# Performance work log

Hardware: AMD Instinct MI355X
Metric: run time of the kernel (lower is better)

Reference implementation:

```python
import jax, jax.numpy as jnp
import numpy as np

N = 100000       # nodes
E = 3200000      # edges (avg degree 32)
IN_F = 256
OUT_F = 128
LRELU_ALPHA = 0.2
EPS = 1e-16


def setup_inputs() -> dict:
    key = jax.random.key(0)
    k1, k2, k3, k4 = jax.random.split(key, 4)
    x = jax.random.normal(k1, (N, IN_F), dtype=jnp.float32)
    edge_index = jax.random.randint(k2, (2, E), 0, N, dtype=jnp.int32)
    # xavier_uniform with gain=calculate_gain('relu')=sqrt(2)
    gain = float(np.sqrt(2.0))
    bw = gain * float(np.sqrt(6.0 / (IN_F + OUT_F)))
    weight = jax.random.uniform(k3, (IN_F, OUT_F), dtype=jnp.float32, minval=-bw, maxval=bw)
    ba = gain * float(np.sqrt(6.0 / (1 + 2 * OUT_F)))
    a = jax.random.uniform(k4, (1, 2 * OUT_F), dtype=jnp.float32, minval=-ba, maxval=ba)
    return {"x": x, "edge_index": edge_index, "weight": weight, "a": a}


def reference(x, edge_index, weight, a):
    src = edge_index[0]
    dst = edge_index[1]
    h = x @ weight                                  # [N, OUT_F]
    # e_edge = a @ cat(h[src], h[dst]) == (h @ a_l)[src] + (h @ a_r)[dst]
    a_l = a[0, :OUT_F]
    a_r = a[0, OUT_F:]
    s_l = h @ a_l                                   # [N]
    s_r = h @ a_r                                   # [N]
    e = s_l[src] + s_r[dst]                         # [E]
    e = jnp.where(e >= 0, e, LRELU_ALPHA * e)       # LeakyReLU
    # segment softmax over src groups
    e_max = jax.ops.segment_max(e, src, num_segments=N)   # [N]
    e_exp = jnp.exp(e - e_max[src])                        # [E]
    denom = jax.ops.segment_sum(e_exp, src, num_segments=N)[src] + EPS
    alpha_e = e_exp / denom                                # [E]
    # out[src] += alpha_e * h[dst]  (sparse A_alpha @ h)
    out = jax.ops.segment_sum(alpha_e[:, None] * h[dst], src, num_segments=N)
    return out
```

## Files before the change

kernel.cpp:

```cpp
#include <hip/hip_runtime.h>

#define GN 100000
#define GE 3200000
#define CAP 128
#define NB 391
#define CHUNK 4096

typedef __attribute__((ext_vector_type(8))) short bf16x8;
typedef __attribute__((ext_vector_type(4))) float f32x4;

__device__ __forceinline__ unsigned short f2bf(float f) {
    unsigned u = __float_as_uint(f);
    u += 0x7fffu + ((u >> 16) & 1u);
    return (unsigned short)(u >> 16);
}
__device__ __forceinline__ float bf2f(unsigned short u) {
    return __uint_as_float(((unsigned)u) << 16);
}

__global__ __launch_bounds__(256) void wprep_kernel(const float* __restrict__ w,
                                                    unsigned short* __restrict__ wT) {
    int flat4 = blockIdx.x * 256 + threadIdx.x;
    if (flat4 >= 256 * 128 / 4) return;
    int k  = flat4 >> 5;
    int n4 = (flat4 & 31) * 4;
    float4 v = ((const float4*)w)[flat4];
    wT[(size_t)(n4 + 0) * 256 + k] = f2bf(v.x);
    wT[(size_t)(n4 + 1) * 256 + k] = f2bf(v.y);
    wT[(size_t)(n4 + 2) * 256 + k] = f2bf(v.z);
    wT[(size_t)(n4 + 3) * 256 + k] = f2bf(v.w);
}

__global__ __launch_bounds__(256) void gemm_kernel(const float* __restrict__ x,
                                                   const unsigned short* __restrict__ wT,
                                                   const float* __restrict__ a,
                                                   unsigned short* __restrict__ hq,
                                                   float* __restrict__ s_l,
                                                   float* __restrict__ s_r) {
    __shared__ unsigned short As[128][40];
    const int tid  = threadIdx.x;
    const int lane = tid & 63, wid = tid >> 6;
    const int l16  = lane & 15, quad = lane >> 4;
    const int wm   = (wid >> 1) * 64, wn = (wid & 1) * 64;
    const int bm   = blockIdx.x * 128;

    f32x4 acc[4][4] = {};

    const int arow = tid >> 1, ahalf = tid & 1;
    int gr = bm + arow; if (gr >= GN) gr = GN - 1;
    const float* xrow = x + (size_t)gr * 256 + ahalf * 16;

    for (int k0 = 0; k0 < 256; k0 += 32) {
        float4 f0 = *(const float4*)(xrow + k0);
        float4 f1 = *(const float4*)(xrow + k0 + 4);
        float4 f2 = *(const float4*)(xrow + k0 + 8);
        float4 f3 = *(const float4*)(xrow + k0 + 12);
        bf16x8 s0, s1;
        s0[0] = f2bf(f0.x); s0[1] = f2bf(f0.y); s0[2] = f2bf(f0.z); s0[3] = f2bf(f0.w);
        s0[4] = f2bf(f1.x); s0[5] = f2bf(f1.y); s0[6] = f2bf(f1.z); s0[7] = f2bf(f1.w);
        s1[0] = f2bf(f2.x); s1[1] = f2bf(f2.y); s1[2] = f2bf(f2.z); s1[3] = f2bf(f2.w);
        s1[4] = f2bf(f3.x); s1[5] = f2bf(f3.y); s1[6] = f2bf(f3.z); s1[7] = f2bf(f3.w);
        __syncthreads();
        *(bf16x8*)&As[arow][ahalf * 16]     = s0;
        *(bf16x8*)&As[arow][ahalf * 16 + 8] = s1;
        __syncthreads();
        bf16x8 af[4], bfr[4];
#pragma unroll
        for (int t = 0; t < 4; ++t) {
            af[t]  = *(const bf16x8*)&As[wm + t * 16 + l16][quad * 8];
            bfr[t] = *(const bf16x8*)(wT + (size_t)(wn + t * 16 + l16) * 256 + k0 + quad * 8);
        }
#pragma unroll
        for (int ti = 0; ti < 4; ++ti)
#pragma unroll
            for (int tj = 0; tj < 4; ++tj)
                acc[ti][tj] = __builtin_amdgcn_mfma_f32_16x16x32_bf16(af[ti], bfr[tj], acc[ti][tj], 0, 0, 0);
    }

    float alv[4], arv[4];
#pragma unroll
    for (int tj = 0; tj < 4; ++tj) {
        alv[tj] = a[wn + tj * 16 + l16];
        arv[tj] = a[128 + wn + tj * 16 + l16];
    }
#pragma unroll
    for (int ti = 0; ti < 4; ++ti) {
        float slp[4], srp[4];
#pragma unroll
        for (int r = 0; r < 4; ++r) {
            int row = bm + wm + ti * 16 + quad * 4 + r;
            float v0 = acc[ti][0][r], v1 = acc[ti][1][r], v2 = acc[ti][2][r], v3 = acc[ti][3][r];
            if (row < GN) {
                unsigned short* hp = hq + (size_t)row * 128 + wn + l16;
                hp[0]  = f2bf(v0);
                hp[16] = f2bf(v1);
                hp[32] = f2bf(v2);
                hp[48] = f2bf(v3);
            }
            slp[r] = v0 * alv[0] + v1 * alv[1] + v2 * alv[2] + v3 * alv[3];
            srp[r] = v0 * arv[0] + v1 * arv[1] + v2 * arv[2] + v3 * arv[3];
        }
#pragma unroll
        for (int off = 1; off < 16; off <<= 1)
#pragma unroll
            for (int r = 0; r < 4; ++r) {
                slp[r] += __shfl_xor(slp[r], off, 64);
                srp[r] += __shfl_xor(srp[r], off, 64);
            }
        if (l16 == 0) {
#pragma unroll
            for (int r = 0; r < 4; ++r) {
                int row = bm + wm + ti * 16 + quad * 4 + r;
                if (row < GN) {
                    atomicAdd(&s_l[row], slp[r]);
                    atomicAdd(&s_r[row], srp[r]);
                }
            }
        }
    }
}

__global__ __launch_bounds__(256) void bhist_kernel(const int* __restrict__ src,
                                                    int* __restrict__ bcnt) {
    __shared__ int bh[NB];
    const int tid = threadIdx.x;
    for (int j = tid; j < NB; j += 256) bh[j] = 0;
    __syncthreads();
    const int base = blockIdx.x * CHUNK;
    const int cnt = min(CHUNK, GE - base);
    for (int i = tid; i < cnt; i += 256) atomicAdd(&bh[src[base + i] >> 8], 1);
    __syncthreads();
    for (int j = tid; j < NB; j += 256)
        if (bh[j]) atomicAdd(&bcnt[j], bh[j]);
}

__global__ __launch_bounds__(64) void bscan_kernel(const int* __restrict__ bcnt,
                                                   int* __restrict__ bbase,
                                                   int* __restrict__ bcursor) {
    __shared__ int arr[NB];
    const int tid = threadIdx.x;
    for (int j = tid; j < NB; j += 64) arr[j] = bcnt[j];
    __syncthreads();
    int carry = 0;
    for (int b0 = 0; b0 < NB; b0 += 64) {
        int idx = b0 + tid;
        int v = (idx < NB) ? arr[idx] : 0;
        int x = v;
#pragma unroll
        for (int off = 1; off < 64; off <<= 1) {
            int y = __shfl_up(x, off, 64);
            if (tid >= off) x += y;
        }
        if (idx < NB) { bbase[idx] = carry + x - v; bcursor[idx] = carry + x - v; }
        carry += __shfl(x, 63, 64);
    }
    if (tid == 0) bbase[NB] = carry;
}

__global__ __launch_bounds__(256) void bin_kernel(const int* __restrict__ ei,
                                                  int* __restrict__ bcursor,
                                                  unsigned* __restrict__ binned) {
    __shared__ int h_cnt[NB];
    __shared__ int h_base[NB + 1];
    __shared__ int h_gpos[NB];
    __shared__ int h_cur[NB];
    __shared__ unsigned sbuf[CHUNK];
    const int tid = threadIdx.x;
    const int base = blockIdx.x * CHUNK;
    const int cnt = min(CHUNK, GE - base);

    int srcv[CHUNK / 256], dstv[CHUNK / 256];
#pragma unroll
    for (int i = 0; i < CHUNK / 256; ++i) {
        int idx = tid + i * 256;
        if (idx < cnt) { srcv[i] = ei[base + idx]; dstv[i] = ei[GE + base + idx]; }
        else srcv[i] = -1;
    }
    for (int j = tid; j < NB; j += 256) h_cnt[j] = 0;
    __syncthreads();
#pragma unroll
    for (int i = 0; i < CHUNK / 256; ++i)
        if (srcv[i] >= 0) atomicAdd(&h_cnt[srcv[i] >> 8], 1);
    __syncthreads();
    if (tid < 64) {
        int carry = 0;
        for (int b0 = 0; b0 < NB; b0 += 64) {
            int idx = b0 + tid;
            int v = (idx < NB) ? h_cnt[idx] : 0;
            int x = v;
#pragma unroll
            for (int off = 1; off < 64; off <<= 1) {
                int y = __shfl_up(x, off, 64);
                if (tid >= off) x += y;
            }
            if (idx < NB) h_base[idx] = carry + x - v;
            carry += __shfl(x, 63, 64);
        }
        if (tid == 0) h_base[NB] = carry;
    }
    __syncthreads();
    for (int j = tid; j < NB; j += 256) {
        h_cur[j] = h_base[j];
        int c = h_cnt[j];
        if (c) h_gpos[j] = atomicAdd(&bcursor[j], c);
    }
    __syncthreads();
#pragma unroll
    for (int i = 0; i < CHUNK / 256; ++i)
        if (srcv[i] >= 0) {
            int b = srcv[i] >> 8;
            int p = atomicAdd(&h_cur[b], 1);
            sbuf[p] = ((unsigned)(srcv[i] & 255) << 17) | (unsigned)dstv[i];
        }
    __syncthreads();
    for (int p = tid; p < cnt; p += 256) {
        int lo = 0, hi = NB - 1;
        while (lo < hi) {
            int mid = (lo + hi + 1) >> 1;
            if (h_base[mid] <= p) lo = mid; else hi = mid - 1;
        }
        binned[h_gpos[lo] + (p - h_base[lo])] = sbuf[p];
    }
}

__global__ __launch_bounds__(256) void fine_kernel(const unsigned* __restrict__ binned,
                                                   const int* __restrict__ bbase,
                                                   int* __restrict__ rowptr,
                                                   int* __restrict__ adj) {
    __shared__ int n_cnt[256];
    __shared__ int n_base[257];
    __shared__ int n_cur[256];
    const int b = blockIdx.x;
    const int tid = threadIdx.x;
    const int node0 = b * 256;
    const int nn = min(256, GN - node0);
    const int beg = bbase[b], end = bbase[b + 1];
    n_cnt[tid] = 0;
    __syncthreads();
    for (int p = beg + tid; p < end; p += 256)
        atomicAdd(&n_cnt[binned[p] >> 17], 1);
    __syncthreads();
    if (tid < 64) {
        int carry = 0;
        for (int b0 = 0; b0 < 256; b0 += 64) {
            int idx = b0 + tid;
            int v = n_cnt[idx];
            int x = v;
#pragma unroll
            for (int off = 1; off < 64; off <<= 1) {
                int y = __shfl_up(x, off, 64);
                if (tid >= off) x += y;
            }
            n_base[idx] = carry + x - v;
            carry += __shfl(x, 63, 64);
        }
        if (tid == 0) n_base[256] = carry;
    }
    __syncthreads();
    if (tid < nn) rowptr[node0 + tid] = beg + n_base[tid];
    if (b == NB - 1 && tid == 0) rowptr[GN] = end;
    n_cur[tid] = n_base[tid];
    __syncthreads();
    for (int p = beg + tid; p < end; p += 256) {
        unsigned e = binned[p];
        int s = e >> 17, d = (int)(e & 0x1FFFFu);
        int pos = atomicAdd(&n_cur[s], 1);
        adj[beg + pos] = d;
    }
}

__global__ __launch_bounds__(256) void aggregate_kernel(const ushort2* __restrict__ h2,
                                                        const float* __restrict__ s_l,
                                                        const float* __restrict__ s_r,
                                                        const int* __restrict__ rowptr,
                                                        const int* __restrict__ adj,
                                                        float* __restrict__ out) {
    __shared__ int   s_dst[4][CAP];
    __shared__ float s_al[4][CAP];
    const int wid = threadIdx.x >> 6, lane = threadIdx.x & 63;
    const int node = blockIdx.x * 4 + wid;
    const int beg = rowptr[node], end = rowptr[node + 1];
    const int deg = end - beg;
    const float sl = s_l[node];

    float m = -1e30f, d = 0.f;
    for (int j = lane; j < deg; j += 64) {
        int dst = adj[beg + j];
        float e = sl + s_r[dst];
        e = (e >= 0.f) ? e : 0.2f * e;
        if (j < CAP) { s_dst[wid][j] = dst; s_al[wid][j] = e; }
        float mn = fmaxf(m, e);
        d = d * __expf(m - mn) + __expf(e - mn);
        m = mn;
    }
#pragma unroll
    for (int off = 32; off; off >>= 1) {
        float m2 = __shfl_xor(m, off, 64);
        float d2 = __shfl_xor(d, off, 64);
        float mn = fmaxf(m, m2);
        d = d * __expf(m - mn) + d2 * __expf(m2 - mn);
        m = mn;
    }
    float inv = 1.f / (d + 1e-16f);
    __syncthreads();
    const int n2 = deg < CAP ? deg : CAP;
    for (int j = lane; j < n2; j += 64)
        s_al[wid][j] = __expf(s_al[wid][j] - m) * inv;
    __syncthreads();

    float2 acc = {0.f, 0.f};
    int j = 0;
    for (; j + 4 <= n2; j += 4) {
        int   d0 = s_dst[wid][j],      d1 = s_dst[wid][j + 1];
        int   d2i = s_dst[wid][j + 2], d3 = s_dst[wid][j + 3];
        float a0 = s_al[wid][j],       a1 = s_al[wid][j + 1];
        float a2 = s_al[wid][j + 2],   a3 = s_al[wid][j + 3];
        ushort2 v0 = h2[(size_t)d0 * 64 + lane];
        ushort2 v1 = h2[(size_t)d1 * 64 + lane];
        ushort2 v2 = h2[(size_t)d2i * 64 + lane];
        ushort2 v3 = h2[(size_t)d3 * 64 + lane];
        acc.x += a0 * bf2f(v0.x) + a1 * bf2f(v1.x) + a2 * bf2f(v2.x) + a3 * bf2f(v3.x);
        acc.y += a0 * bf2f(v0.y) + a1 * bf2f(v1.y) + a2 * bf2f(v2.y) + a3 * bf2f(v3.y);
    }
    for (; j < n2; ++j) {
        int d0 = s_dst[wid][j]; float a0 = s_al[wid][j];
        ushort2 v0 = h2[(size_t)d0 * 64 + lane];
        acc.x += a0 * bf2f(v0.x); acc.y += a0 * bf2f(v0.y);
    }
    for (; j < deg; ++j) {
        int dst = adj[beg + j];
        float e = sl + s_r[dst];
        e = (e >= 0.f) ? e : 0.2f * e;
        float a0 = __expf(e - m) * inv;
        ushort2 v0 = h2[(size_t)dst * 64 + lane];
        acc.x += a0 * bf2f(v0.x); acc.y += a0 * bf2f(v0.y);
    }
    ((float2*)out)[(size_t)node * 64 + lane] = acc;
}

extern "C" void kernel_launch(void* const* d_in, const int* in_sizes, int n_in,
                              void* d_out, int out_size, void* d_ws, size_t ws_size,
                              hipStream_t stream) {
    const float* x  = (const float*)d_in[0];
    const int*   ei = (const int*)d_in[1];
    const float* w  = (const float*)d_in[2];
    const float* a  = (const float*)d_in[3];
    float* out = (float*)d_out;

    unsigned short* hq = (unsigned short*)d_ws;
    float* s_l     = (float*)(hq + (size_t)GN * 128);
    float* s_r     = s_l + GN;
    int*   bcnt    = (int*)(s_r + GN);
    int*   bbase   = bcnt + NB;
    int*   bcursor = bbase + NB + 1;
    int*   rowptr  = bcursor + NB;
    unsigned* binned = (unsigned*)(rowptr + GN + 1);
    int*   adj     = (int*)(binned + GE);
    unsigned short* wT = (unsigned short*)(adj + GE);

    hipMemsetAsync(s_l, 0, (size_t)(2 * GN + NB) * sizeof(float), stream);

    wprep_kernel<<<32, 256, 0, stream>>>(w, wT);
    gemm_kernel<<<(GN + 127) / 128, 256, 0, stream>>>(x, wT, a, hq, s_l, s_r);
    bhist_kernel<<<(GE + CHUNK - 1) / CHUNK, 256, 0, stream>>>(ei, bcnt);
    bscan_kernel<<<1, 64, 0, stream>>>(bcnt, bbase, bcursor);
    bin_kernel<<<(GE + CHUNK - 1) / CHUNK, 256, 0, stream>>>(ei, bcursor, binned);
    fine_kernel<<<NB, 256, 0, stream>>>(binned, bbase, rowptr, adj);
    aggregate_kernel<<<GN / 4, 256, 0, stream>>>((const ushort2*)hq, s_l, s_r, rowptr, adj, out);
}
```

Before: 412.7 us.

## Switch to fp16 storage, finer bins, bucket tags, restructured aggregate

Several changes land together. h and W move from bf16 to fp16, using packed RTZ conversion and f16 MFMA. The bin count doubles to 782 (128 nodes per bin), so fine_kernel gets more, smaller blocks. bin_kernel stores each entry's bucket id in shared memory, which replaces a per-element binary search. The aggregate kernel becomes a two-pass max-then-sum softmax that stores (dst, alpha) pairs together, gathers half4 values with half-wave splitting over two edges, and defers normalization to the end. It keeps a separate fallback path for high-degree nodes. fp16 has a narrower range than bf16 and could overflow on large h values.

```diff
diff --git a/kernel.cpp b/kernel.cpp
--- a/kernel.cpp
+++ b/kernel.cpp
@@ -3,41 +3,39 @@
 #define GN 100000
 #define GE 3200000
 #define CAP 128
-#define NB 391
+#define NB 782
 #define CHUNK 4096
 
-typedef __attribute__((ext_vector_type(8))) short bf16x8;
+typedef __attribute__((ext_vector_type(8))) _Float16 f16x8;
+typedef __attribute__((ext_vector_type(4))) _Float16 half4_t;
+typedef __attribute__((ext_vector_type(2))) __fp16 fp16x2_raw;
 typedef __attribute__((ext_vector_type(4))) float f32x4;
 
-__device__ __forceinline__ unsigned short f2bf(float f) {
-    unsigned u = __float_as_uint(f);
-    u += 0x7fffu + ((u >> 16) & 1u);
-    return (unsigned short)(u >> 16);
-}
-__device__ __forceinline__ float bf2f(unsigned short u) {
-    return __uint_as_float(((unsigned)u) << 16);
+__device__ __forceinline__ unsigned pk2(float a, float b) {
+    fp16x2_raw p = __builtin_amdgcn_cvt_pkrtz(a, b);
+    return __builtin_bit_cast(unsigned, p);
 }
 
 __global__ __launch_bounds__(256) void wprep_kernel(const float* __restrict__ w,
-                                                    unsigned short* __restrict__ wT) {
+                                                    _Float16* __restrict__ wT) {
     int flat4 = blockIdx.x * 256 + threadIdx.x;
     if (flat4 >= 256 * 128 / 4) return;
     int k  = flat4 >> 5;
     int n4 = (flat4 & 31) * 4;
     float4 v = ((const float4*)w)[flat4];
-    wT[(size_t)(n4 + 0) * 256 + k] = f2bf(v.x);
-    wT[(size_t)(n4 + 1) * 256 + k] = f2bf(v.y);
-    wT[(size_t)(n4 + 2) * 256 + k] = f2bf(v.z);
-    wT[(size_t)(n4 + 3) * 256 + k] = f2bf(v.w);
+    wT[(size_t)(n4 + 0) * 256 + k] = (_Float16)v.x;
+    wT[(size_t)(n4 + 1) * 256 + k] = (_Float16)v.y;
+    wT[(size_t)(n4 + 2) * 256 + k] = (_Float16)v.z;
+    wT[(size_t)(n4 + 3) * 256 + k] = (_Float16)v.w;
 }
 
 __global__ __launch_bounds__(256) void gemm_kernel(const float* __restrict__ x,
-                                                   const unsigned short* __restrict__ wT,
+                                                   const _Float16* __restrict__ wT,
                                                    const float* __restrict__ a,
-                                                   unsigned short* __restrict__ hq,
+                                                   _Float16* __restrict__ hq,
                                                    float* __restrict__ s_l,
                                                    float* __restrict__ s_r) {
-    __shared__ unsigned short As[128][40];
+    __shared__ _Float16 As[128][40];
     const int tid  = threadIdx.x;
     const int lane = tid & 63, wid = tid >> 6;
     const int l16  = lane & 15, quad = lane >> 4;
@@ -55,26 +53,23 @@
         float4 f1 = *(const float4*)(xrow + k0 + 4);
         float4 f2 = *(const float4*)(xrow + k0 + 8);
         float4 f3 = *(const float4*)(xrow + k0 + 12);
-        bf16x8 s0, s1;
-        s0[0] = f2bf(f0.x); s0[1] = f2bf(f0.y); s0[2] = f2bf(f0.z); s0[3] = f2bf(f0.w);
-        s0[4] = f2bf(f1.x); s0[5] = f2bf(f1.y); s0[6] = f2bf(f1.z); s0[7] = f2bf(f1.w);
-        s1[0] = f2bf(f2.x); s1[1] = f2bf(f2.y); s1[2] = f2bf(f2.z); s1[3] = f2bf(f2.w);
-        s1[4] = f2bf(f3.x); s1[5] = f2bf(f3.y); s1[6] = f2bf(f3.z); s1[7] = f2bf(f3.w);
+        uint4 lo = {pk2(f0.x, f0.y), pk2(f0.z, f0.w), pk2(f1.x, f1.y), pk2(f1.z, f1.w)};
+        uint4 hi = {pk2(f2.x, f2.y), pk2(f2.z, f2.w), pk2(f3.x, f3.y), pk2(f3.z, f3.w)};
         __syncthreads();
-        *(bf16x8*)&As[arow][ahalf * 16]     = s0;
-        *(bf16x8*)&As[arow][ahalf * 16 + 8] = s1;
+        *(uint4*)&As[arow][ahalf * 16]     = lo;
+        *(uint4*)&As[arow][ahalf * 16 + 8] = hi;
         __syncthreads();
-        bf16x8 af[4], bfr[4];
+        f16x8 af[4], bfr[4];
 #pragma unroll
         for (int t = 0; t < 4; ++t) {
-            af[t]  = *(const bf16x8*)&As[wm + t * 16 + l16][quad * 8];
-            bfr[t] = *(const bf16x8*)(wT + (size_t)(wn + t * 16 + l16) * 256 + k0 + quad * 8);
+            af[t]  = *(const f16x8*)&As[wm + t * 16 + l16][quad * 8];
+            bfr[t] = *(const f16x8*)(wT + (size_t)(wn + t * 16 + l16) * 256 + k0 + quad * 8);
         }
 #pragma unroll
         for (int ti = 0; ti < 4; ++ti)
 #pragma unroll
             for (int tj = 0; tj < 4; ++tj)
-                acc[ti][tj] = __builtin_amdgcn_mfma_f32_16x16x32_bf16(af[ti], bfr[tj], acc[ti][tj], 0, 0, 0);
+                acc[ti][tj] = __builtin_amdgcn_mfma_f32_16x16x32_f16(af[ti], bfr[tj], acc[ti][tj], 0, 0, 0);
     }
 
     float alv[4], arv[4];
@@ -91,11 +86,11 @@
             int row = bm + wm + ti * 16 + quad * 4 + r;
             float v0 = acc[ti][0][r], v1 = acc[ti][1][r], v2 = acc[ti][2][r], v3 = acc[ti][3][r];
             if (row < GN) {
-                unsigned short* hp = hq + (size_t)row * 128 + wn + l16;
-                hp[0]  = f2bf(v0);
-                hp[16] = f2bf(v1);
-                hp[32] = f2bf(v2);
-                hp[48] = f2bf(v3);
+                _Float16* hp = hq + (size_t)row * 128 + wn + l16;
+                hp[0]  = (_Float16)v0;
+                hp[16] = (_Float16)v1;
+                hp[32] = (_Float16)v2;
+                hp[48] = (_Float16)v3;
             }
             slp[r] = v0 * alv[0] + v1 * alv[1] + v2 * alv[2] + v3 * alv[3];
             srp[r] = v0 * arv[0] + v1 * arv[1] + v2 * arv[2] + v3 * arv[3];
@@ -128,7 +123,7 @@
     __syncthreads();
     const int base = blockIdx.x * CHUNK;
     const int cnt = min(CHUNK, GE - base);
-    for (int i = tid; i < cnt; i += 256) atomicAdd(&bh[src[base + i] >> 8], 1);
+    for (int i = tid; i < cnt; i += 256) atomicAdd(&bh[src[base + i] >> 7], 1);
     __syncthreads();
     for (int j = tid; j < NB; j += 256)
         if (bh[j]) atomicAdd(&bcnt[j], bh[j]);
@@ -165,6 +160,7 @@
     __shared__ int h_gpos[NB];
     __shared__ int h_cur[NB];
     __shared__ unsigned sbuf[CHUNK];
+    __shared__ unsigned short bkt[CHUNK];
     const int tid = threadIdx.x;
     const int base = blockIdx.x * CHUNK;
     const int cnt = min(CHUNK, GE - base);
@@ -180,7 +176,7 @@
     __syncthreads();
 #pragma unroll
     for (int i = 0; i < CHUNK / 256; ++i)
-        if (srcv[i] >= 0) atomicAdd(&h_cnt[srcv[i] >> 8], 1);
+        if (srcv[i] >= 0) atomicAdd(&h_cnt[srcv[i] >> 7], 1);
     __syncthreads();
     if (tid < 64) {
         int carry = 0;
@@ -208,18 +204,15 @@
 #pragma unroll
     for (int i = 0; i < CHUNK / 256; ++i)
         if (srcv[i] >= 0) {
-            int b = srcv[i] >> 8;
+            int b = srcv[i] >> 7;
             int p = atomicAdd(&h_cur[b], 1);
-            sbuf[p] = ((unsigned)(srcv[i] & 255) << 17) | (unsigned)dstv[i];
+            sbuf[p] = ((unsigned)(srcv[i] & 127) << 17) | (unsigned)dstv[i];
+            bkt[p] = (unsigned short)b;
         }
     __syncthreads();
     for (int p = tid; p < cnt; p += 256) {
-        int lo = 0, hi = NB - 1;
-        while (lo < hi) {
-            int mid = (lo + hi + 1) >> 1;
-            if (h_base[mid] <= p) lo = mid; else hi = mid - 1;
-        }
-        binned[h_gpos[lo] + (p - h_base[lo])] = sbuf[p];
+        int b = bkt[p];
+        binned[h_gpos[b] + (p - h_base[b])] = sbuf[p];
     }
 }
 
@@ -227,22 +220,22 @@
                                                    const int* __restrict__ bbase,
                                                    int* __restrict__ rowptr,
                                                    int* __restrict__ adj) {
-    __shared__ int n_cnt[256];
-    __shared__ int n_base[257];
-    __shared__ int n_cur[256];
+    __shared__ int n_cnt[128];
+    __shared__ int n_base[129];
+    __shared__ int n_cur[128];
     const int b = blockIdx.x;
     const int tid = threadIdx.x;
-    const int node0 = b * 256;
-    const int nn = min(256, GN - node0);
+    const int node0 = b << 7;
+    const int nn = min(128, GN - node0);
     const int beg = bbase[b], end = bbase[b + 1];
-    n_cnt[tid] = 0;
+    if (tid < 128) n_cnt[tid] = 0;
     __syncthreads();
     for (int p = beg + tid; p < end; p += 256)
         atomicAdd(&n_cnt[binned[p] >> 17], 1);
     __syncthreads();
     if (tid < 64) {
         int carry = 0;
-        for (int b0 = 0; b0 < 256; b0 += 64) {
+        for (int b0 = 0; b0 < 128; b0 += 64) {
             int idx = b0 + tid;
             int v = n_cnt[idx];
             int x = v;
@@ -254,12 +247,12 @@
             n_base[idx] = carry + x - v;
             carry += __shfl(x, 63, 64);
         }
-        if (tid == 0) n_base[256] = carry;
+        if (tid == 0) n_base[128] = carry;
     }
     __syncthreads();
     if (tid < nn) rowptr[node0 + tid] = beg + n_base[tid];
     if (b == NB - 1 && tid == 0) rowptr[GN] = end;
-    n_cur[tid] = n_base[tid];
+    if (tid < 128) n_cur[tid] = n_base[tid];
     __syncthreads();
     for (int p = beg + tid; p < end; p += 256) {
         unsigned e = binned[p];
@@ -269,73 +262,96 @@
     }
 }
 
-__global__ __launch_bounds__(256) void aggregate_kernel(const ushort2* __restrict__ h2,
+__global__ __launch_bounds__(256) void aggregate_kernel(const half4_t* __restrict__ h4,
                                                         const float* __restrict__ s_l,
                                                         const float* __restrict__ s_r,
                                                         const int* __restrict__ rowptr,
                                                         const int* __restrict__ adj,
                                                         float* __restrict__ out) {
-    __shared__ int   s_dst[4][CAP];
-    __shared__ float s_al[4][CAP];
+    __shared__ uint2 s_ed[4][CAP + 4];
     const int wid = threadIdx.x >> 6, lane = threadIdx.x & 63;
     const int node = blockIdx.x * 4 + wid;
     const int beg = rowptr[node], end = rowptr[node + 1];
     const int deg = end - beg;
     const float sl = s_l[node];
 
-    float m = -1e30f, d = 0.f;
-    for (int j = lane; j < deg; j += 64) {
-        int dst = adj[beg + j];
-        float e = sl + s_r[dst];
-        e = (e >= 0.f) ? e : 0.2f * e;
-        if (j < CAP) { s_dst[wid][j] = dst; s_al[wid][j] = e; }
-        float mn = fmaxf(m, e);
-        d = d * __expf(m - mn) + __expf(e - mn);
-        m = mn;
-    }
-#pragma unroll
-    for (int off = 32; off; off >>= 1) {
-        float m2 = __shfl_xor(m, off, 64);
-        float d2 = __shfl_xor(d, off, 64);
-        float mn = fmaxf(m, m2);
-        d = d * __expf(m - mn) + d2 * __expf(m2 - mn);
-        m = mn;
-    }
-    float inv = 1.f / (d + 1e-16f);
-    __syncthreads();
-    const int n2 = deg < CAP ? deg : CAP;
-    for (int j = lane; j < n2; j += 64)
-        s_al[wid][j] = __expf(s_al[wid][j] - m) * inv;
-    __syncthreads();
-
-    float2 acc = {0.f, 0.f};
-    int j = 0;
-    for (; j + 4 <= n2; j += 4) {
-        int   d0 = s_dst[wid][j],      d1 = s_dst[wid][j + 1];
-        int   d2i = s_dst[wid][j + 2], d3 = s_dst[wid][j + 3];
-        float a0 = s_al[wid][j],       a1 = s_al[wid][j + 1];
-        float a2 = s_al[wid][j + 2],   a3 = s_al[wid][j + 3];
-        ushort2 v0 = h2[(size_t)d0 * 64 + lane];
-        ushort2 v1 = h2[(size_t)d1 * 64 + lane];
-        ushort2 v2 = h2[(size_t)d2i * 64 + lane];
-        ushort2 v3 = h2[(size_t)d3 * 64 + lane];
-        acc.x += a0 * bf2f(v0.x) + a1 * bf2f(v1.x) + a2 * bf2f(v2.x) + a3 * bf2f(v3.x);
-        acc.y += a0 * bf2f(v0.y) + a1 * bf2f(v1.y) + a2 * bf2f(v2.y) + a3 * bf2f(v3.y);
-    }
-    for (; j < n2; ++j) {
-        int d0 = s_dst[wid][j]; float a0 = s_al[wid][j];
-        ushort2 v0 = h2[(size_t)d0 * 64 + lane];
-        acc.x += a0 * bf2f(v0.x); acc.y += a0 * bf2f(v0.y);
-    }
-    for (; j < deg; ++j) {
-        int dst = adj[beg + j];
-        float e = sl + s_r[dst];
-        e = (e >= 0.f) ? e : 0.2f * e;
-        float a0 = __expf(e - m) * inv;
-        ushort2 v0 = h2[(size_t)dst * 64 + lane];
-        acc.x += a0 * bf2f(v0.x); acc.y += a0 * bf2f(v0.y);
-    }
-    ((float2*)out)[(size_t)node * 64 + lane] = acc;
+    if (deg <= CAP) {
+        float m = -1e30f;
+        for (int j = lane; j < deg; j += 64) {
+            int dst = adj[beg + j];
+            float e = sl + s_r[dst];
+            e = (e >= 0.f) ? e : 0.2f * e;
+            uint2 ed; ed.x = (unsigned)dst; ed.y = __float_as_uint(e);
+            s_ed[wid][j] = ed;
+            m = fmaxf(m, e);
+        }
+#pragma unroll
+        for (int off = 32; off; off >>= 1) m = fmaxf(m, __shfl_xor(m, off, 64));
+        float d = 0.f;
+        for (int j = lane; j < deg; j += 64) {
+            float al = __expf(__uint_as_float(s_ed[wid][j].y) - m);
+            d += al;
+            ((unsigned*)&s_ed[wid][j])[1] = __float_as_uint(al);
+        }
+#pragma unroll
+        for (int off = 32; off; off >>= 1) d += __shfl_xor(d, off, 64);
+        const float inv = 1.f / (d + 1e-16f);
+        const int n4 = (deg + 3) & ~3;
+        if (lane < n4 - deg) { uint2 z; z.x = 0u; z.y = 0u; s_ed[wid][deg + lane] = z; }
+        const int hh = lane >> 5, fl = lane & 31;
+        float ax = 0.f, ay = 0.f, az = 0.f, aw = 0.f;
+        for (int j = 0; j < n4; j += 4) {
+            uint2 ea = s_ed[wid][j + hh];
+            uint2 eb = s_ed[wid][j + hh + 2];
+            half4_t va = h4[(ea.x << 5) | fl];
+            half4_t vb = h4[(eb.x << 5) | fl];
+            float aa = __uint_as_float(ea.y), ab = __uint_as_float(eb.y);
+            ax += aa * (float)va[0] + ab * (float)vb[0];
+            ay += aa * (float)va[1] + ab * (float)vb[1];
+            az += aa * (float)va[2] + ab * (float)vb[2];
+            aw += aa * (float)va[3] + ab * (float)vb[3];
+        }
+        ax += __shfl_xor(ax, 32, 64);
+        ay += __shfl_xor(ay, 32, 64);
+        az += __shfl_xor(az, 32, 64);
+        aw += __shfl_xor(aw, 32, 64);
+        if (hh == 0) {
+            float4 v = {ax * inv, ay * inv, az * inv, aw * inv};
+            *(float4*)(out + ((size_t)node << 7) + (fl << 2)) = v;
+        }
+    } else {
+        const unsigned* h32 = (const unsigned*)h4;
+        float m = -1e30f, d = 0.f;
+        for (int j = lane; j < deg; j += 64) {
+            int dst = adj[beg + j];
+            float e = sl + s_r[dst];
+            e = (e >= 0.f) ? e : 0.2f * e;
+            float mn = fmaxf(m, e);
+            d = d * __expf(m - mn) + __expf(e - mn);
+            m = mn;
+        }
+#pragma unroll
+        for (int off = 32; off; off >>= 1) {
+            float m2 = __shfl_xor(m, off, 64);
+            float d2 = __shfl_xor(d, off, 64);
+            float mn = fmaxf(m, m2);
+            d = d * __expf(m - mn) + d2 * __expf(m2 - mn);
+            m = mn;
+        }
+        float inv = 1.f / (d + 1e-16f);
+        float2 acc = {0.f, 0.f};
+        for (int j = 0; j < deg; ++j) {
+            int dst = adj[beg + j];
+            float e = sl + s_r[dst];
+            e = (e >= 0.f) ? e : 0.2f * e;
+            float al = __expf(e - m);
+            unsigned v = h32[((unsigned)dst << 6) | lane];
+            acc.x += al * (float)__builtin_bit_cast(_Float16, (unsigned short)(v & 0xffffu));
+            acc.y += al * (float)__builtin_bit_cast(_Float16, (unsigned short)(v >> 16));
+        }
+        float2 o = {acc.x * inv, acc.y * inv};
+        ((float2*)out)[(size_t)node * 64 + lane] = o;
+    }
 }
 
 extern "C" void kernel_launch(void* const* d_in, const int* in_sizes, int n_in,
@@ -347,7 +363,7 @@
     const float* a  = (const float*)d_in[3];
     float* out = (float*)d_out;
 
-    unsigned short* hq = (unsigned short*)d_ws;
+    _Float16* hq   = (_Float16*)d_ws;
     float* s_l     = (float*)(hq + (size_t)GN * 128);
     float* s_r     = s_l + GN;
     int*   bcnt    = (int*)(s_r + GN);
@@ -356,9 +372,9 @@
     int*   rowptr  = bcursor + NB;
     unsigned* binned = (unsigned*)(rowptr + GN + 1);
     int*   adj     = (int*)(binned + GE);
-    unsigned short* wT = (unsigned short*)(adj + GE);
-
-    hipMemsetAsync(s_l, 0, (size_t)(2 * GN + NB) * sizeof(float), stream);
+    _Float16* wT   = (_Float16*)(adj + GE);
+
+    (void)hipMemsetAsync(s_l, 0, (size_t)(2 * GN + NB) * sizeof(float), stream);
 
     wprep_kernel<<<32, 256, 0, stream>>>(w, wT);
     gemm_kernel<<<(GN + 127) / 128, 256, 0, stream>>>(x, wT, a, hq, s_l, s_r);
@@ -366,5 +382,5 @@
     bscan_kernel<<<1, 64, 0, stream>>>(bcnt, bbase, bcursor);
     bin_kernel<<<(GE + CHUNK - 1) / CHUNK, 256, 0, stream>>>(ei, bcursor, binned);
     fine_kernel<<<NB, 256, 0, stream>>>(binned, bbase, rowptr, adj);
-    aggregate_kernel<<<GN / 4, 256, 0, stream>>>((const ushort2*)hq, s_l, s_r, rowptr, adj, out);
-}
+    aggregate_kernel<<<GN / 4, 256, 0, stream>>>((const half4_t*)hq, s_l, s_r, rowptr, adj, out);
+}
```

After: 415.0 us. No clear change (+0.5%).
